# Kernel optimization log

Hardware: AMD Instinct MI355X
Metric: run time of the kernel (lower is better)

The kernel has to match this reference:

```python
import jax, jax.numpy as jnp
import numpy as np

QUALITY_ALPHA = 1.0
TOPK = 4
MIX_BETA = 0.5
NEG = -1e9


def setup_inputs() -> dict:
    key = jax.random.key(0)
    ks = jax.random.split(key, 12)
    B, S, D, H, Q, QH = 64, 2048, 512, 128, 4, 32
    feats = jax.random.normal(ks[0], (B, S, D), dtype=jnp.float32)
    mask = jax.random.uniform(ks[1], (B, S)) > 0.3
    mask = mask.at[:, 0].set(True)  # guarantee >=1 valid segment per row
    seg_quality = jax.random.normal(ks[2], (B, S, Q), dtype=jnp.float32)
    W1 = jax.random.normal(ks[3], (D, H), dtype=jnp.float32) * 0.05
    b1 = jnp.zeros((H,), dtype=jnp.float32)
    w2 = jax.random.normal(ks[4], (H, 1), dtype=jnp.float32) * 0.05
    b2 = jnp.zeros((1,), dtype=jnp.float32)
    qW1 = jax.random.normal(ks[5], (Q, QH), dtype=jnp.float32) * 0.05
    qb1 = jnp.zeros((QH,), dtype=jnp.float32)
    qw2 = jax.random.normal(ks[6], (QH, 1), dtype=jnp.float32) * 0.05
    qb2 = jnp.zeros((1,), dtype=jnp.float32)
    return dict(feats=feats, mask=mask, seg_quality=seg_quality,
                W1=W1, b1=b1, w2=w2, b2=b2, qW1=qW1, qb1=qb1, qw2=qw2, qb2=qb2)


def _masked_softmax(logits, mask):
    logits = jnp.where(mask, logits, NEG)
    w = jax.nn.softmax(logits, axis=1)
    w = w * mask.astype(w.dtype)
    return w / jnp.maximum(w.sum(axis=1, keepdims=True), 1e-8)


def reference(feats, mask, seg_quality, W1, b1, w2, b2, qW1, qb1, qw2, qb2):
    # evidence scorer: Linear -> tanh -> Linear  ([B,S,D] -> [B,S])
    evidence = (jnp.tanh(jnp.einsum('bsd,dh->bsh', feats, W1) + b1) @ w2)[..., 0] + b2[0]
    # quality net: Linear -> relu -> Linear  ([B,S,Q] -> [B,S])
    quality = (jax.nn.relu(jnp.einsum('bsq,qh->bsh', seg_quality, qW1) + qb1) @ qw2)[..., 0] + qb2[0]
    combined = evidence + QUALITY_ALPHA * quality

    weights = _masked_softmax(combined, mask)
    attn_pooled = jnp.einsum('bsd,bs->bd', feats, weights)

    # top-k path on combined logits
    masked_scores = jnp.where(mask, combined, NEG)
    _, topk_indices = jax.lax.top_k(masked_scores, TOPK)          # [B, k]
    topk_feats = jnp.take_along_axis(feats, topk_indices[..., None], axis=1)  # [B, k, D]
    topk_valid = jnp.take_along_axis(mask, topk_indices, axis=1)  # [B, k] bool
    denom = jnp.maximum(topk_valid.astype(feats.dtype).sum(axis=1, keepdims=True), 1.0)
    topk_pooled = (topk_feats * topk_valid[..., None].astype(feats.dtype)).sum(axis=1) / denom

    pooled = MIX_BETA * attn_pooled + (1.0 - MIX_BETA) * topk_pooled
    return pooled, weights, attn_pooled, topk_pooled, topk_indices, topk_valid
```

## Files before the change

### kernel.cpp

```cpp
#include <hip/hip_runtime.h>
#include <cstdint>
#include <cstddef>

#define B 64
#define S 2048
#define D 512
#define H 128
#define Q 4
#define QH 32
#define KTOP 4
#define NROWS (B * S)
#define NEGV -1e9f
#define NCH 32
#define SC (S / NCH)

typedef __bf16 bf16x8 __attribute__((ext_vector_type(8)));
typedef float f32x4 __attribute__((ext_vector_type(4)));
typedef unsigned short us8 __attribute__((ext_vector_type(8)));

__device__ __forceinline__ unsigned hasbyte(unsigned v, unsigned c) {
    unsigned x = v ^ (c * 0x01010101u);
    return (x - 0x01010101u) & ~x & 0x80808080u;
}

__device__ __forceinline__ void split_f32(float x, unsigned short& hi, unsigned short& lo) {
    unsigned bx = __float_as_uint(x);
    hi = (unsigned short)(bx >> 16);
    float fh = __uint_as_float(bx & 0xFFFF0000u);
    lo = (unsigned short)(__float_as_uint(x - fh) >> 16);
}

__device__ __forceinline__ float tanh_f(float x) {
    float e = __expf(2.f * x);
    return 1.f - __fdividef(2.f, e + 1.f);
}

__device__ __forceinline__ void gll16(const void* g, void* l) {
    __builtin_amdgcn_global_load_lds(
        (const __attribute__((address_space(1))) unsigned int*)g,
        (__attribute__((address_space(3))) unsigned int*)l, 16, 0, 0);
}

__global__ __launch_bounds__(256) void prep_kernel(
    const float* __restrict__ W1, unsigned short* __restrict__ bh,
    unsigned short* __restrict__ bl, const unsigned char* __restrict__ m,
    int* __restrict__ mode) {
    const int t = threadIdx.x;
    if (blockIdx.x < 256) {
        int i = blockIdx.x * 256 + t;
        int h = i >> 9, k = i & 511;
        float x = W1[(size_t)k * H + h];
        unsigned short hv, lv;
        split_f32(x, hv, lv);
        bh[i] = hv;
        bl[i] = lv;
        return;
    }
    __shared__ int fF0, fF, fB, fO4;
    if (t == 0) { fF0 = 0; fF = 0; fB = 0; fO4 = 0; }
    __syncthreads();
    const uint4* mv = (const uint4*)m;
    int a = 0, bb = 0, c = 0, d = 0;
    for (int i = t; i < NROWS / 16; i += 256) {
        uint4 v = mv[i];
        if (hasbyte(v.x, 0xF0u) | hasbyte(v.y, 0xF0u) | hasbyte(v.z, 0xF0u) | hasbyte(v.w, 0xF0u)) a = 1;
        if (hasbyte(v.x, 0x3Fu) | hasbyte(v.y, 0x3Fu) | hasbyte(v.z, 0x3Fu) | hasbyte(v.w, 0x3Fu) |
            hasbyte(v.x, 0x80u) | hasbyte(v.y, 0x80u) | hasbyte(v.z, 0x80u) | hasbyte(v.w, 0x80u)) bb = 1;
        if ((v.x & 0xFFFFFF00u) | (v.y & 0xFFFFFF00u) | (v.z & 0xFFFFFF00u) | (v.w & 0xFFFFFF00u)) c = 1;
        if ((v.y & 0xFFu) | (v.w & 0xFFu)) d = 1;
    }
    if (a) atomicOr(&fF0, 1);
    if (bb) atomicOr(&fF, 1);
    if (c) atomicOr(&fB, 1);
    if (d) atomicOr(&fO4, 1);
    __syncthreads();
    if (t == 0) {
        int md;
        if (fF0) md = 4;
        else if (fF) md = 3;
        else if (fB) md = 0;
        else if (fO4) md = 1;
        else md = 2;
        *mode = md;
    }
}

__global__ __launch_bounds__(512, 4) void evidence_kernel(
    const float* __restrict__ feats, const unsigned short* __restrict__ wbh,
    const unsigned short* __restrict__ wbl, const float* __restrict__ b1g,
    const float* __restrict__ w2g, const float* __restrict__ b2g,
    const void* __restrict__ mraw, const int* __restrict__ mode,
    const float* __restrict__ segq, const float* __restrict__ qW1,
    const float* __restrict__ qb1, const float* __restrict__ qw2,
    const float* __restrict__ qb2, float* __restrict__ comb,
    float* __restrict__ ew, float* __restrict__ Zpart) {
    __shared__ unsigned short sAh[128][40];
    __shared__ unsigned short sAl[128][40];
    __shared__ unsigned short sBh[128][32];
    __shared__ unsigned short sBl[128][32];
    __shared__ float red[128][2];
    __shared__ float sew[128];
    __shared__ float sQW[Q * QH];
    __shared__ float sQb1[QH];
    __shared__ float sQw2[QH];
    __shared__ float sQb2;

    const int t = threadIdx.x;
    const int lane = t & 63;
    const int wid = t >> 6;
    const int wm = wid >> 1;
    const int wn = wid & 1;
    const int l16 = lane & 15, lk = lane >> 4;
    const int row0 = blockIdx.x * 128;
    const int md = *mode;

    if (t < Q * QH) sQW[t] = qW1[t];
    else if (t < 160) sQb1[t - 128] = qb1[t - 128];
    else if (t < 192) sQw2[t - 160] = qw2[t - 160];
    else if (t == 192) sQb2 = qb2[0];

    f32x4 acc[2][4];
#pragma unroll
    for (int mf = 0; mf < 2; ++mf)
#pragma unroll
        for (int nf = 0; nf < 4; ++nf) acc[mf][nf] = (f32x4)0.f;

    const int ar = t >> 2;
    const int ak = (t & 3) * 8;
    const float* fsrc = feats + (size_t)(row0 + ar) * D + ak;

    const int bhr = t >> 2;
    const int bslot = (t & 3) ^ ((t >> 3) & 3);
    const unsigned short* bsrc_h = wbh + (size_t)bhr * D + bslot * 8;
    const unsigned short* bsrc_l = wbl + (size_t)bhr * D + bslot * 8;
    char* dstBh = (char*)&sBh[0][0] + wid * 1024;
    char* dstBl = (char*)&sBl[0][0] + wid * 1024;

    for (int kc = 0; kc < D; kc += 32) {
        gll16(bsrc_h + kc, dstBh);
        gll16(bsrc_l + kc, dstBl);

        float f[8];
        *reinterpret_cast<float4*>(&f[0]) = *reinterpret_cast<const float4*>(fsrc + kc + 0);
        *reinterpret_cast<float4*>(&f[4]) = *reinterpret_cast<const float4*>(fsrc + kc + 4);
        us8 vh, vl;
#pragma unroll
        for (int j = 0; j < 8; ++j) {
            unsigned short hh, ll;
            split_f32(f[j], hh, ll);
            vh[j] = hh; vl[j] = ll;
        }
        *reinterpret_cast<us8*>(&sAh[ar][ak]) = vh;
        *reinterpret_cast<us8*>(&sAl[ar][ak]) = vl;

        __syncthreads();

        bf16x8 ah[2], al[2], bh[4], bl[4];
#pragma unroll
        for (int mf = 0; mf < 2; ++mf) {
            int rr = wm * 32 + mf * 16 + l16;
            ah[mf] = *reinterpret_cast<const bf16x8*>(&sAh[rr][lk * 8]);
            al[mf] = *reinterpret_cast<const bf16x8*>(&sAl[rr][lk * 8]);
        }
#pragma unroll
        for (int nf = 0; nf < 4; ++nf) {
            int hh = wn * 64 + nf * 16 + l16;
            int sp = (lk ^ ((hh >> 1) & 3)) * 8;
            bh[nf] = *reinterpret_cast<const bf16x8*>(&sBh[hh][sp]);
            bl[nf] = *reinterpret_cast<const bf16x8*>(&sBl[hh][sp]);
        }
#pragma unroll
        for (int mf = 0; mf < 2; ++mf)
#pragma unroll
            for (int nf = 0; nf < 4; ++nf) {
                acc[mf][nf] = __builtin_amdgcn_mfma_f32_16x16x32_bf16(ah[mf], bh[nf], acc[mf][nf], 0, 0, 0);
                acc[mf][nf] = __builtin_amdgcn_mfma_f32_16x16x32_bf16(ah[mf], bl[nf], acc[mf][nf], 0, 0, 0);
                acc[mf][nf] = __builtin_amdgcn_mfma_f32_16x16x32_bf16(al[mf], bh[nf], acc[mf][nf], 0, 0, 0);
            }
        __syncthreads();
    }

    float b1v[4], w2v[4];
#pragma unroll
    for (int nf = 0; nf < 4; ++nf) {
        int hh = wn * 64 + nf * 16 + l16;
        b1v[nf] = b1g[hh];
        w2v[nf] = w2g[hh];
    }
#pragma unroll
    for (int mf = 0; mf < 2; ++mf)
#pragma unroll
        for (int r2 = 0; r2 < 4; ++r2) {
            float s = 0.f;
#pragma unroll
            for (int nf = 0; nf < 4; ++nf) s += tanh_f(acc[mf][nf][r2] + b1v[nf]) * w2v[nf];
            s += __shfl_xor(s, 1, 16);
            s += __shfl_xor(s, 2, 16);
            s += __shfl_xor(s, 4, 16);
            s += __shfl_xor(s, 8, 16);
            if (l16 == 0) red[wm * 32 + mf * 16 + lk * 4 + r2][wn] = s;
        }
    __syncthreads();

    if (t < 128) {
        const int row = row0 + t;
        float4 sq = *reinterpret_cast<const float4*>(&segq[(size_t)row * Q]);
        float q = sQb2;
#pragma unroll
        for (int h = 0; h < QH; ++h) {
            float a = sq.x * sQW[h] + sq.y * sQW[QH + h] + sq.z * sQW[2 * QH + h] + sq.w * sQW[3 * QH + h] + sQb1[h];
            q += fmaxf(a, 0.f) * sQw2[h];
        }
        float mv;
        switch (md) {
            case 0: mv = ((const unsigned char*)mraw)[row] ? 1.f : 0.f; break;
            case 1: mv = ((const int*)mraw)[row] ? 1.f : 0.f; break;
            case 2: mv = ((const long long*)mraw)[row] ? 1.f : 0.f; break;
            case 3: mv = (((const float*)mraw)[row] != 0.f) ? 1.f : 0.f; break;
            default: mv = (((const double*)mraw)[row] != 0.0) ? 1.f : 0.f; break;
        }
        float e = red[t][0] + red[t][1] + b2g[0];
        float c = (mv != 0.f) ? (e + q) : NEGV;
        comb[row] = c;
        float x = __expf(c);
        ew[row] = x;
        sew[t] = x;
    }
    __syncthreads();
    if (t < 64) {
        float z = sew[t] + sew[t + 64];
#pragma unroll
        for (int o = 32; o > 0; o >>= 1) z += __shfl_xor(z, o, 64);
        if (t == 0) Zpart[blockIdx.x] = z;
    }
}

__global__ __launch_bounds__(256) void pool_partial_kernel(
    const float* __restrict__ feats, const float* __restrict__ ew, float* __restrict__ part) {
    const int ch = (NCH - 1) - blockIdx.x;
    const int b = (B - 1) - blockIdx.y;
    const int t = threadIdx.x;
    const int s0 = ch * SC;
    __shared__ float sw[SC];
    __shared__ float4 redp[256];
    if (t < SC) sw[t] = ew[(size_t)b * S + s0 + t];
    __syncthreads();
    const int dq = (t & 127) * 4;
    const int rp = t >> 7;
    float4 a = {0.f, 0.f, 0.f, 0.f};
    const float* fp = feats + ((size_t)b * S + s0 + rp) * D + dq;
#pragma unroll 8
    for (int s = rp; s < SC; s += 2) {
        float wv = sw[s];
        if (wv != 0.f) {
            float4 f = *reinterpret_cast<const float4*>(fp);
            a.x += wv * f.x; a.y += wv * f.y; a.z += wv * f.z; a.w += wv * f.w;
        }
        fp += 2 * D;
    }
    redp[t] = a;
    __syncthreads();
    if (t < 128) {
        float4 o = redp[t], o2 = redp[t + 128];
        o.x += o2.x; o.y += o2.y; o.z += o2.z; o.w += o2.w;
        *reinterpret_cast<float4*>(&part[((size_t)(b * NCH + ch)) * D + dq]) = o;
    }
}

__global__ __launch_bounds__(256) void finalize_kernel(
    const float* __restrict__ comb, const float* __restrict__ Zpart,
    const float* __restrict__ part, const float* __restrict__ feats,
    float* __restrict__ o_weights, float* __restrict__ o_tidx, float* __restrict__ o_tval,
    float* __restrict__ o_attn, float* __restrict__ o_topk, float* __restrict__ o_pooled) {
    __shared__ float sc[S];
    __shared__ float sinv;
    __shared__ float mvv[256 * 4];
    __shared__ int mii[256 * 4];
    __shared__ int sti[4];
    __shared__ float stv[4];
    __shared__ float sdn;
    const int b = blockIdx.x, t = threadIdx.x;
    const float* row = comb + (size_t)b * S;

    if (t == 0) {
        float z = 0.f;
#pragma unroll
        for (int j = 0; j < 16; ++j) z += Zpart[b * 16 + j];
        sinv = 1.f / fmaxf(z, 1e-8f);
    }
    __syncthreads();
    const float inv = sinv;

    float tv[4] = {-3e38f, -3e38f, -3e38f, -3e38f};
    int ti[4] = {1 << 30, 1 << 30, 1 << 30, 1 << 30};
    for (int s = t; s < S; s += 256) {
        float v = row[s];
        sc[s] = v;
        o_weights[(size_t)b * S + s] = __expf(v) * inv;
        if (v > tv[3]) {
            tv[3] = v; ti[3] = s;
#pragma unroll
            for (int k = 3; k > 0; --k) {
                bool up = (tv[k] > tv[k - 1]) || (tv[k] == tv[k - 1] && ti[k] < ti[k - 1]);
                if (up) {
                    float fv = tv[k]; tv[k] = tv[k - 1]; tv[k - 1] = fv;
                    int ii = ti[k]; ti[k] = ti[k - 1]; ti[k - 1] = ii;
                }
            }
        }
    }
#pragma unroll
    for (int k = 0; k < 4; ++k) { mvv[t * 4 + k] = tv[k]; mii[t * 4 + k] = ti[k]; }
    __syncthreads();
    for (int st = 128; st >= 1; st >>= 1) {
        if (t < st) {
            float av[4], bv[4];
            int ai[4], bi[4];
#pragma unroll
            for (int k = 0; k < 4; ++k) {
                av[k] = mvv[t * 4 + k]; ai[k] = mii[t * 4 + k];
                bv[k] = mvv[(t + st) * 4 + k]; bi[k] = mii[(t + st) * 4 + k];
            }
            float rv[4]; int ri[4];
            int i = 0, j = 0;
            for (int o = 0; o < 4; ++o) {
                bool ta = (av[i] > bv[j]) || (av[i] == bv[j] && ai[i] < bi[j]);
                if (ta) { rv[o] = av[i]; ri[o] = ai[i]; ++i; }
                else { rv[o] = bv[j]; ri[o] = bi[j]; ++j; }
            }
#pragma unroll
            for (int k = 0; k < 4; ++k) { mvv[t * 4 + k] = rv[k]; mii[t * 4 + k] = ri[k]; }
        }
        __syncthreads();
    }
    if (t == 0) {
        float dn = 0.f;
#pragma unroll
        for (int k = 0; k < 4; ++k) {
            int idx = mii[k];
            int valid = (mvv[k] > -1e8f) ? 1 : 0;
            sti[k] = idx;
            stv[k] = (float)valid;
            o_tidx[b * 4 + k] = (float)idx;
            o_tval[b * 4 + k] = (float)valid;
            dn += (float)valid;
        }
        sdn = fmaxf(dn, 1.f);
    }
    __syncthreads();

    const int i0 = sti[0], i1 = sti[1], i2 = sti[2], i3 = sti[3];
    const float v0 = stv[0], v1 = stv[1], v2 = stv[2], v3 = stv[3];
    const float inv_dn = 1.f / sdn;
    for (int d = t; d < D; d += 256) {
        float s = 0.f;
#pragma unroll
        for (int ch = 0; ch < NCH; ++ch) s += part[((size_t)(b * NCH + ch)) * D + d];
        s *= inv;
        float tk = v0 * feats[((size_t)b * S + i0) * D + d] + v1 * feats[((size_t)b * S + i1) * D + d] +
                   v2 * feats[((size_t)b * S + i2) * D + d] + v3 * feats[((size_t)b * S + i3) * D + d];
        tk *= inv_dn;
        o_attn[(size_t)b * D + d] = s;
        o_topk[(size_t)b * D + d] = tk;
        o_pooled[(size_t)b * D + d] = 0.5f * s + 0.5f * tk;
    }
}

extern "C" void kernel_launch(void* const* d_in, const int* in_sizes, int n_in,
                              void* d_out, int out_size, void* d_ws, size_t ws_size,
                              hipStream_t stream) {
    const float* feats = (const float*)d_in[0];
    const void* maskraw = d_in[1];
    const float* segq = (const float*)d_in[2];
    const float* W1 = (const float*)d_in[3];
    const float* b1 = (const float*)d_in[4];
    const float* w2 = (const float*)d_in[5];
    const float* b2 = (const float*)d_in[6];
    const float* qW1 = (const float*)d_in[7];
    const float* qb1 = (const float*)d_in[8];
    const float* qw2 = (const float*)d_in[9];
    const float* qb2 = (const float*)d_in[10];

    char* ws = (char*)d_ws;
    int* mode = (int*)ws;
    float* comb = (float*)(ws + 16);
    float* ewb = comb + NROWS;
    float* part = ewb + NROWS;
    float* Zpart = part + (size_t)B * NCH * D;
    unsigned short* wsBh = (unsigned short*)(Zpart + 1024);
    unsigned short* wsBl = wsBh + (size_t)H * D;

    float* out = (float*)d_out;
    float* o_pooled = out;
    float* o_weights = out + (size_t)B * D;
    float* o_attn = o_weights + (size_t)B * S;
    float* o_topk = o_attn + (size_t)B * D;
    float* o_tidx = o_topk + (size_t)B * D;
    float* o_tval = o_tidx + (size_t)B * KTOP;

    prep_kernel<<<257, 256, 0, stream>>>(W1, wsBh, wsBl, (const unsigned char*)maskraw, mode);
    evidence_kernel<<<NROWS / 128, 512, 0, stream>>>(
        feats, wsBh, wsBl, b1, w2, b2, maskraw, mode, segq, qW1, qb1, qw2, qb2,
        comb, ewb, Zpart);
    pool_partial_kernel<<<dim3(NCH, B), 256, 0, stream>>>(feats, ewb, part);
    finalize_kernel<<<B, 256, 0, stream>>>(comb, Zpart, part, feats, o_weights,
                                           o_tidx, o_tval, o_attn, o_topk, o_pooled);
}
```

Measured before the change: 152.7 us.

## Fuse attention pooling into evidence GEMM kernel using LDS-resident bf16 feats

Removes the separate pool_partial kernel. The evidence kernel now keeps all 16 k-chunks of the bf16-high feature tile in LDS and computes per-block weighted partial sums from it. This avoids a second full read of feats from HBM. It also replaces global_load_lds with register prefetch of the next k-chunk and switches the hi/lo split to round-to-nearest. The trade-offs: a large LDS footprint that limits occupancy to about one block per CU, and pooling computed from bf16-rounded features, which reduces precision.

```diff
diff --git a/kernel.cpp b/kernel.cpp
--- a/kernel.cpp
+++ b/kernel.cpp
@@ -11,8 +11,9 @@
 #define KTOP 4
 #define NROWS (B * S)
 #define NEGV -1e9f
-#define NCH 32
-#define SC (S / NCH)
+#define RPB 128
+#define NBLK (NROWS / RPB)
+#define CPB (S / RPB)
 
 typedef __bf16 bf16x8 __attribute__((ext_vector_type(8)));
 typedef float f32x4 __attribute__((ext_vector_type(4)));
@@ -23,22 +24,21 @@
     return (x - 0x01010101u) & ~x & 0x80808080u;
 }
 
-__device__ __forceinline__ void split_f32(float x, unsigned short& hi, unsigned short& lo) {
-    unsigned bx = __float_as_uint(x);
-    hi = (unsigned short)(bx >> 16);
-    float fh = __uint_as_float(bx & 0xFFFF0000u);
-    lo = (unsigned short)(__float_as_uint(x - fh) >> 16);
+__device__ __forceinline__ unsigned short rnbf(float x) {
+    unsigned u = __float_as_uint(x);
+    unsigned r = u + 0x7FFFu + ((u >> 16) & 1u);
+    return (unsigned short)(r >> 16);
+}
+
+__device__ __forceinline__ void split_rn(float x, unsigned short& hi, unsigned short& lo) {
+    hi = rnbf(x);
+    float fh = __uint_as_float((unsigned)hi << 16);
+    lo = rnbf(x - fh);
 }
 
 __device__ __forceinline__ float tanh_f(float x) {
     float e = __expf(2.f * x);
     return 1.f - __fdividef(2.f, e + 1.f);
-}
-
-__device__ __forceinline__ void gll16(const void* g, void* l) {
-    __builtin_amdgcn_global_load_lds(
-        (const __attribute__((address_space(1))) unsigned int*)g,
-        (__attribute__((address_space(3))) unsigned int*)l, 16, 0, 0);
 }
 
 __global__ __launch_bounds__(256) void prep_kernel(
@@ -51,7 +51,7 @@
         int h = i >> 9, k = i & 511;
         float x = W1[(size_t)k * H + h];
         unsigned short hv, lv;
-        split_f32(x, hv, lv);
+        split_rn(x, hv, lv);
         bh[i] = hv;
         bl[i] = lv;
         return;
@@ -85,7 +85,7 @@
     }
 }
 
-__global__ __launch_bounds__(512, 4) void evidence_kernel(
+__global__ __launch_bounds__(512) void fused_kernel(
     const float* __restrict__ feats, const unsigned short* __restrict__ wbh,
     const unsigned short* __restrict__ wbl, const float* __restrict__ b1g,
     const float* __restrict__ w2g, const float* __restrict__ b2g,
@@ -93,13 +93,13 @@
     const float* __restrict__ segq, const float* __restrict__ qW1,
     const float* __restrict__ qb1, const float* __restrict__ qw2,
     const float* __restrict__ qb2, float* __restrict__ comb,
-    float* __restrict__ ew, float* __restrict__ Zpart) {
-    __shared__ unsigned short sAh[128][40];
-    __shared__ unsigned short sAl[128][40];
-    __shared__ unsigned short sBh[128][32];
-    __shared__ unsigned short sBl[128][32];
-    __shared__ float red[128][2];
-    __shared__ float sew[128];
+    float* __restrict__ Zpart, float* __restrict__ part) {
+    __shared__ unsigned short Ah[16][RPB][32];
+    __shared__ unsigned short Al[RPB][32];
+    __shared__ unsigned short Bh[H][32];
+    __shared__ unsigned short Bl[H][32];
+    __shared__ float red[RPB][2];
+    __shared__ float sew[RPB];
     __shared__ float sQW[Q * QH];
     __shared__ float sQb1[QH];
     __shared__ float sQw2[QH];
@@ -111,7 +111,7 @@
     const int wm = wid >> 1;
     const int wn = wid & 1;
     const int l16 = lane & 15, lk = lane >> 4;
-    const int row0 = blockIdx.x * 128;
+    const int row0 = blockIdx.x * RPB;
     const int md = *mode;
 
     if (t < Q * QH) sQW[t] = qW1[t];
@@ -119,55 +119,62 @@
     else if (t < 192) sQw2[t - 160] = qw2[t - 160];
     else if (t == 192) sQb2 = qb2[0];
 
+    const int ar = t >> 2;
+    const int o = t & 3;
+    const int po = o ^ ((ar >> 1) & 3);
+    const float* fsrc = feats + (size_t)(row0 + ar) * D + o * 8;
+    const unsigned short* bsrch = wbh + (size_t)ar * D + o * 8;
+    const unsigned short* bsrcl = wbl + (size_t)ar * D + o * 8;
+
     f32x4 acc[2][4];
 #pragma unroll
     for (int mf = 0; mf < 2; ++mf)
 #pragma unroll
         for (int nf = 0; nf < 4; ++nf) acc[mf][nf] = (f32x4)0.f;
 
-    const int ar = t >> 2;
-    const int ak = (t & 3) * 8;
-    const float* fsrc = feats + (size_t)(row0 + ar) * D + ak;
-
-    const int bhr = t >> 2;
-    const int bslot = (t & 3) ^ ((t >> 3) & 3);
-    const unsigned short* bsrc_h = wbh + (size_t)bhr * D + bslot * 8;
-    const unsigned short* bsrc_l = wbl + (size_t)bhr * D + bslot * 8;
-    char* dstBh = (char*)&sBh[0][0] + wid * 1024;
-    char* dstBl = (char*)&sBl[0][0] + wid * 1024;
-
-    for (int kc = 0; kc < D; kc += 32) {
-        gll16(bsrc_h + kc, dstBh);
-        gll16(bsrc_l + kc, dstBl);
-
-        float f[8];
-        *reinterpret_cast<float4*>(&f[0]) = *reinterpret_cast<const float4*>(fsrc + kc + 0);
-        *reinterpret_cast<float4*>(&f[4]) = *reinterpret_cast<const float4*>(fsrc + kc + 4);
+    float rA[8];
+    us8 rBh, rBl;
+    *reinterpret_cast<float4*>(&rA[0]) = *reinterpret_cast<const float4*>(fsrc + 0);
+    *reinterpret_cast<float4*>(&rA[4]) = *reinterpret_cast<const float4*>(fsrc + 4);
+    rBh = *reinterpret_cast<const us8*>(bsrch);
+    rBl = *reinterpret_cast<const us8*>(bsrcl);
+    {
         us8 vh, vl;
 #pragma unroll
         for (int j = 0; j < 8; ++j) {
             unsigned short hh, ll;
-            split_f32(f[j], hh, ll);
+            split_rn(rA[j], hh, ll);
             vh[j] = hh; vl[j] = ll;
         }
-        *reinterpret_cast<us8*>(&sAh[ar][ak]) = vh;
-        *reinterpret_cast<us8*>(&sAl[ar][ak]) = vl;
-
+        *reinterpret_cast<us8*>(&Ah[0][ar][po * 8]) = vh;
+        *reinterpret_cast<us8*>(&Al[ar][po * 8]) = vl;
+        *reinterpret_cast<us8*>(&Bh[ar][po * 8]) = rBh;
+        *reinterpret_cast<us8*>(&Bl[ar][po * 8]) = rBl;
+    }
+
+    for (int kci = 0; kci < 16; ++kci) {
         __syncthreads();
-
+        if (kci < 15) {
+            const int kc = (kci + 1) * 32;
+            *reinterpret_cast<float4*>(&rA[0]) = *reinterpret_cast<const float4*>(fsrc + kc);
+            *reinterpret_cast<float4*>(&rA[4]) = *reinterpret_cast<const float4*>(fsrc + kc + 4);
+            rBh = *reinterpret_cast<const us8*>(bsrch + kc);
+            rBl = *reinterpret_cast<const us8*>(bsrcl + kc);
+        }
         bf16x8 ah[2], al[2], bh[4], bl[4];
 #pragma unroll
         for (int mf = 0; mf < 2; ++mf) {
             int rr = wm * 32 + mf * 16 + l16;
-            ah[mf] = *reinterpret_cast<const bf16x8*>(&sAh[rr][lk * 8]);
-            al[mf] = *reinterpret_cast<const bf16x8*>(&sAl[rr][lk * 8]);
+            int sp = (lk ^ ((rr >> 1) & 3)) * 8;
+            ah[mf] = *reinterpret_cast<const bf16x8*>(&Ah[kci][rr][sp]);
+            al[mf] = *reinterpret_cast<const bf16x8*>(&Al[rr][sp]);
         }
 #pragma unroll
         for (int nf = 0; nf < 4; ++nf) {
             int hh = wn * 64 + nf * 16 + l16;
             int sp = (lk ^ ((hh >> 1) & 3)) * 8;
-            bh[nf] = *reinterpret_cast<const bf16x8*>(&sBh[hh][sp]);
-            bl[nf] = *reinterpret_cast<const bf16x8*>(&sBl[hh][sp]);
+            bh[nf] = *reinterpret_cast<const bf16x8*>(&Bh[hh][sp]);
+            bl[nf] = *reinterpret_cast<const bf16x8*>(&Bl[hh][sp]);
         }
 #pragma unroll
         for (int mf = 0; mf < 2; ++mf)
@@ -178,6 +185,19 @@
                 acc[mf][nf] = __builtin_amdgcn_mfma_f32_16x16x32_bf16(al[mf], bh[nf], acc[mf][nf], 0, 0, 0);
             }
         __syncthreads();
+        if (kci < 15) {
+            us8 vh, vl;
+#pragma unroll
+            for (int j = 0; j < 8; ++j) {
+                unsigned short hh, ll;
+                split_rn(rA[j], hh, ll);
+                vh[j] = hh; vl[j] = ll;
+            }
+            *reinterpret_cast<us8*>(&Ah[kci + 1][ar][po * 8]) = vh;
+            *reinterpret_cast<us8*>(&Al[ar][po * 8]) = vl;
+            *reinterpret_cast<us8*>(&Bh[ar][po * 8]) = rBh;
+            *reinterpret_cast<us8*>(&Bl[ar][po * 8]) = rBl;
+        }
     }
 
     float b1v[4], w2v[4];
@@ -202,7 +222,7 @@
         }
     __syncthreads();
 
-    if (t < 128) {
+    if (t < RPB) {
         const int row = row0 + t;
         float4 sq = *reinterpret_cast<const float4*>(&segq[(size_t)row * Q]);
         float q = sQb2;
@@ -222,48 +242,36 @@
         float e = red[t][0] + red[t][1] + b2g[0];
         float c = (mv != 0.f) ? (e + q) : NEGV;
         comb[row] = c;
-        float x = __expf(c);
-        ew[row] = x;
-        sew[t] = x;
-    }
-    __syncthreads();
+        sew[t] = __expf(c);
+    }
+    __syncthreads();
+
     if (t < 64) {
         float z = sew[t] + sew[t + 64];
 #pragma unroll
-        for (int o = 32; o > 0; o >>= 1) z += __shfl_xor(z, o, 64);
+        for (int oo = 32; oo > 0; oo >>= 1) z += __shfl_xor(z, oo, 64);
         if (t == 0) Zpart[blockIdx.x] = z;
     }
-}
-
-__global__ __launch_bounds__(256) void pool_partial_kernel(
-    const float* __restrict__ feats, const float* __restrict__ ew, float* __restrict__ part) {
-    const int ch = (NCH - 1) - blockIdx.x;
-    const int b = (B - 1) - blockIdx.y;
-    const int t = threadIdx.x;
-    const int s0 = ch * SC;
-    __shared__ float sw[SC];
-    __shared__ float4 redp[256];
-    if (t < SC) sw[t] = ew[(size_t)b * S + s0 + t];
-    __syncthreads();
-    const int dq = (t & 127) * 4;
-    const int rp = t >> 7;
-    float4 a = {0.f, 0.f, 0.f, 0.f};
-    const float* fp = feats + ((size_t)b * S + s0 + rp) * D + dq;
+
+    if (t < 256) {
+        const int d0 = t * 2;
+        const int kci = d0 >> 5;
+        const int c = d0 & 31;
+        const int og = c >> 3, c7 = c & 7;
+        float a0 = 0.f, a1 = 0.f;
 #pragma unroll 8
-    for (int s = rp; s < SC; s += 2) {
-        float wv = sw[s];
-        if (wv != 0.f) {
-            float4 f = *reinterpret_cast<const float4*>(fp);
-            a.x += wv * f.x; a.y += wv * f.y; a.z += wv * f.z; a.w += wv * f.w;
-        }
-        fp += 2 * D;
-    }
-    redp[t] = a;
-    __syncthreads();
-    if (t < 128) {
-        float4 o = redp[t], o2 = redp[t + 128];
-        o.x += o2.x; o.y += o2.y; o.z += o2.z; o.w += o2.w;
-        *reinterpret_cast<float4*>(&part[((size_t)(b * NCH + ch)) * D + dq]) = o;
+        for (int r = 0; r < RPB; ++r) {
+            const int row = (r + kci) & (RPB - 1);
+            const int sp = (og ^ ((row >> 1) & 3)) * 8 + c7;
+            unsigned v = *reinterpret_cast<const unsigned*>(&Ah[kci][row][sp]);
+            float f0 = __uint_as_float((v & 0xFFFFu) << 16);
+            float f1 = __uint_as_float(v & 0xFFFF0000u);
+            float w = sew[row];
+            a0 += w * f0;
+            a1 += w * f1;
+        }
+        float2 o2 = make_float2(a0, a1);
+        *reinterpret_cast<float2*>(&part[(size_t)blockIdx.x * D + d0]) = o2;
     }
 }
 
@@ -272,7 +280,6 @@
     const float* __restrict__ part, const float* __restrict__ feats,
     float* __restrict__ o_weights, float* __restrict__ o_tidx, float* __restrict__ o_tval,
     float* __restrict__ o_attn, float* __restrict__ o_topk, float* __restrict__ o_pooled) {
-    __shared__ float sc[S];
     __shared__ float sinv;
     __shared__ float mvv[256 * 4];
     __shared__ int mii[256 * 4];
@@ -285,7 +292,7 @@
     if (t == 0) {
         float z = 0.f;
 #pragma unroll
-        for (int j = 0; j < 16; ++j) z += Zpart[b * 16 + j];
+        for (int j = 0; j < CPB; ++j) z += Zpart[b * CPB + j];
         sinv = 1.f / fmaxf(z, 1e-8f);
     }
     __syncthreads();
@@ -295,7 +302,6 @@
     int ti[4] = {1 << 30, 1 << 30, 1 << 30, 1 << 30};
     for (int s = t; s < S; s += 256) {
         float v = row[s];
-        sc[s] = v;
         o_weights[(size_t)b * S + s] = __expf(v) * inv;
         if (v > tv[3]) {
             tv[3] = v; ti[3] = s;
@@ -323,10 +329,10 @@
             }
             float rv[4]; int ri[4];
             int i = 0, j = 0;
-            for (int o = 0; o < 4; ++o) {
+            for (int oo = 0; oo < 4; ++oo) {
                 bool ta = (av[i] > bv[j]) || (av[i] == bv[j] && ai[i] < bi[j]);
-                if (ta) { rv[o] = av[i]; ri[o] = ai[i]; ++i; }
-                else { rv[o] = bv[j]; ri[o] = bi[j]; ++j; }
+                if (ta) { rv[oo] = av[i]; ri[oo] = ai[i]; ++i; }
+                else { rv[oo] = bv[j]; ri[oo] = bi[j]; ++j; }
             }
 #pragma unroll
             for (int k = 0; k < 4; ++k) { mvv[t * 4 + k] = rv[k]; mii[t * 4 + k] = ri[k]; }
@@ -355,7 +361,7 @@
     for (int d = t; d < D; d += 256) {
         float s = 0.f;
 #pragma unroll
-        for (int ch = 0; ch < NCH; ++ch) s += part[((size_t)(b * NCH + ch)) * D + d];
+        for (int ch = 0; ch < CPB; ++ch) s += part[((size_t)(b * CPB + ch)) * D + d];
         s *= inv;
         float tk = v0 * feats[((size_t)b * S + i0) * D + d] + v1 * feats[((size_t)b * S + i1) * D + d] +
                    v2 * feats[((size_t)b * S + i2) * D + d] + v3 * feats[((size_t)b * S + i3) * D + d];
@@ -384,10 +390,9 @@
     char* ws = (char*)d_ws;
     int* mode = (int*)ws;
     float* comb = (float*)(ws + 16);
-    float* ewb = comb + NROWS;
-    float* part = ewb + NROWS;
-    float* Zpart = part + (size_t)B * NCH * D;
-    unsigned short* wsBh = (unsigned short*)(Zpart + 1024);
+    float* part = comb + NROWS;
+    float* Zpart = part + (size_t)NBLK * D;
+    unsigned short* wsBh = (unsigned short*)(Zpart + NBLK);
     unsigned short* wsBl = wsBh + (size_t)H * D;
 
     float* out = (float*)d_out;
@@ -399,10 +404,9 @@
     float* o_tval = o_tidx + (size_t)B * KTOP;
 
     prep_kernel<<<257, 256, 0, stream>>>(W1, wsBh, wsBl, (const unsigned char*)maskraw, mode);
-    evidence_kernel<<<NROWS / 128, 512, 0, stream>>>(
+    fused_kernel<<<NBLK, 512, 0, stream>>>(
         feats, wsBh, wsBl, b1, w2, b2, maskraw, mode, segq, qW1, qb1, qw2, qb2,
-        comb, ewb, Zpart);
-    pool_partial_kernel<<<dim3(NCH, B), 256, 0, stream>>>(feats, ewb, part);
+        comb, Zpart, part);
     finalize_kernel<<<B, 256, 0, stream>>>(comb, Zpart, part, feats, o_weights,
                                            o_tidx, o_tval, o_attn, o_topk, o_pooled);
 }
```

Result: slower. 162.8 us (+6.7%).
